# Optimization experiments

Measured on AMD Instinct MI355X. Metric: run time of the kernel, lower is better.

Reference implementation:

```python
import jax, jax.numpy as jnp
import numpy as np

N_NODES = 50000
N_EDGES = 800000
IN_DIM = 16
HID = 128
OUT_DIM = 1
N_LAYERS = 2


def setup_inputs() -> dict:
    key = jax.random.key(0)
    ks = jax.random.split(key, 16)
    s = 0.05
    inp = {
        "edge_feats": jax.random.normal(ks[0], (N_EDGES, IN_DIM), jnp.float32),
        "node_feats": jax.random.normal(ks[1], (N_NODES, 4), jnp.float32),
        "src": jax.random.randint(ks[2], (N_EDGES,), 0, N_NODES, jnp.int32),
        "dst": jax.random.randint(ks[3], (N_EDGES,), 0, N_NODES, jnp.int32),
        # edge_embedding (dead in original forward, kept for faithfulness)
        "W_eemb": jax.random.normal(ks[4], (IN_DIM, HID), jnp.float32) * s,
        "b_eemb": jnp.zeros((HID,), jnp.float32),
        # node_embedding: Linear(4, hidden)
        "W_nemb": jax.random.normal(ks[5], (4, HID), jnp.float32) * s,
        "b_nemb": jnp.zeros((HID,), jnp.float32),
        # stacked GraphConv weights [n_layers, H, H]
        "gnn_W": jax.random.normal(ks[6], (N_LAYERS, HID, HID), jnp.float32) * s,
        "gnn_b": jnp.zeros((N_LAYERS, HID), jnp.float32),
        # output MLP
        "out_W1": jax.random.normal(ks[7], (HID, HID), jnp.float32) * s,
        "out_b1": jnp.zeros((HID,), jnp.float32),
        "out_W2": jax.random.normal(ks[8], (HID, OUT_DIM), jnp.float32) * s,
        "out_b2": jnp.zeros((OUT_DIM,), jnp.float32),
    }
    return inp


def reference(edge_feats, node_feats, src, dst, W_eemb, b_eemb, W_nemb, b_nemb,
              gnn_W, gnn_b, out_W1, out_b1, out_W2, out_b2):
    ones = jnp.ones((src.shape[0],), jnp.float32)
    deg_out = jnp.clip(jax.ops.segment_sum(ones, src, num_segments=N_NODES), 1.0)
    deg_in = jnp.clip(jax.ops.segment_sum(ones, dst, num_segments=N_NODES), 1.0)
    norm_out = deg_out ** -0.5  # [N]
    norm_in = deg_in ** -0.5    # [N]

    # edge_embedding output is dead code in the original forward (overwritten)
    _h_e = edge_feats @ W_eemb + b_eemb

    h = node_feats @ W_nemb + b_nemb  # [N, H]
    for l in range(N_LAYERS):
        # DGL GraphConv norm='both': D_out^{-1/2} gather -> scatter-sum -> D_in^{-1/2} -> W, b
        hs = h * norm_out[:, None]
        agg = jax.ops.segment_sum(hs[src], dst, num_segments=N_NODES)  # [N, H]
        h = agg * norm_in[:, None]
        h = h @ gnn_W[l] + gnn_b[l]
        h = jax.nn.relu(h)

    edge_h = h[src] + h[dst]  # apply_edges UDF, [E, H]
    x = jax.nn.relu(edge_h @ out_W1 + out_b1)
    return x @ out_W2 + out_b2  # [E, OUT_DIM]
```

## Files before the change

kernel.cpp:

```cpp
#include <hip/hip_runtime.h>

#define N_NODES 50000
#define N_EDGES 800000
#define HID 128
#define NB 256
#define NPB 196
#define TP 136

typedef __attribute__((ext_vector_type(8))) short bf16x8;
typedef __attribute__((ext_vector_type(4))) float f32x4;

__device__ __forceinline__ unsigned pack2bf(float a, float b) {
  unsigned ua = __float_as_uint(a);
  ua += 0x7FFFu + ((ua >> 16) & 1u);
  unsigned ub = __float_as_uint(b);
  ub += 0x7FFFu + ((ub >> 16) & 1u);
  return (ua >> 16) | (ub & 0xFFFF0000u);
}
#define BFLO(u) __uint_as_float((u) << 16)
#define BFHI(u) __uint_as_float((u) & 0xFFFF0000u)


__global__ __launch_bounds__(256) void p1_hist_kernel(
    const int* __restrict__ src, const int* __restrict__ dst,
    int* __restrict__ bcnt_d, int* __restrict__ bcnt_s) {
  __shared__ int hd[NB], hs[NB];
  int t = threadIdx.x;
  hd[t] = 0; hs[t] = 0;
  __syncthreads();
  for (int e = blockIdx.x * 256 + t; e < N_EDGES; e += gridDim.x * 256) {
    atomicAdd(&hd[dst[e] / NPB], 1);
    atomicAdd(&hs[src[e] / NPB], 1);
  }
  __syncthreads();
  if (hd[t]) atomicAdd(&bcnt_d[t], hd[t]);
  if (hs[t]) atomicAdd(&bcnt_s[t], hs[t]);
}

__global__ void p2_scan_kernel(const int* __restrict__ bcnt_d, const int* __restrict__ bcnt_s,
                               int* __restrict__ bofs_d, int* __restrict__ bofs_s,
                               int* __restrict__ cur_d, int* __restrict__ cur_s) {
  __shared__ int s[NB];
  int t = threadIdx.x;
  int v = bcnt_d[t];
  s[t] = v;
  __syncthreads();
  for (int o = 1; o < NB; o <<= 1) {
    int x = (t >= o) ? s[t - o] : 0;
    __syncthreads();
    s[t] += x;
    __syncthreads();
  }
  int ofs = s[t] - v;
  bofs_d[t] = ofs; cur_d[t] = ofs;
  if (t == NB - 1) bofs_d[NB] = s[t];
  __syncthreads();
  v = bcnt_s[t];
  s[t] = v;
  __syncthreads();
  for (int o = 1; o < NB; o <<= 1) {
    int x = (t >= o) ? s[t - o] : 0;
    __syncthreads();
    s[t] += x;
    __syncthreads();
  }
  ofs = s[t] - v;
  bofs_s[t] = ofs; cur_s[t] = ofs;
  if (t == NB - 1) bofs_s[NB] = s[t];
}

__global__ __launch_bounds__(256) void p3_scatter_dst_kernel(
    const int* __restrict__ src, const int* __restrict__ dst,
    int* __restrict__ cur_d, int2* __restrict__ sdst) {
  __shared__ int bcnt[NB], bbase[NB];
  int t = threadIdx.x;
  int base = blockIdx.x * 2048;
  bcnt[t] = 0;
  __syncthreads();
  int myb[8], myr[8], mys[8], myp[8];
#pragma unroll
  for (int u = 0; u < 8; ++u) {
    int e = base + u * 256 + t;
    myb[u] = -1;
    if (e < N_EDGES) {
      int d = dst[e];
      int b = d / NPB;
      myb[u] = b;
      myr[u] = atomicAdd(&bcnt[b], 1);
      mys[u] = src[e];
      myp[u] = ((d - b * NPB) << 20) | e;
    }
  }
  __syncthreads();
  int c = bcnt[t];
  if (c) bbase[t] = atomicAdd(&cur_d[t], c);
  __syncthreads();
#pragma unroll
  for (int u = 0; u < 8; ++u) {
    if (myb[u] >= 0) sdst[bbase[myb[u]] + myr[u]] = make_int2(mys[u], myp[u]);
  }
}

__global__ __launch_bounds__(256) void p3_scatter_src_kernel(
    const int* __restrict__ src, int* __restrict__ cur_s, int* __restrict__ ssrc) {
  __shared__ int bcnt[NB], bbase[NB];
  int t = threadIdx.x;
  int base = blockIdx.x * 2048;
  bcnt[t] = 0;
  __syncthreads();
  int myb[8], myr[8], mys[8];
#pragma unroll
  for (int u = 0; u < 8; ++u) {
    int e = base + u * 256 + t;
    myb[u] = -1;
    if (e < N_EDGES) {
      int s = src[e];
      int b = s / NPB;
      myb[u] = b;
      myr[u] = atomicAdd(&bcnt[b], 1);
      mys[u] = s;
    }
  }
  __syncthreads();
  int c = bcnt[t];
  if (c) bbase[t] = atomicAdd(&cur_s[t], c);
  __syncthreads();
#pragma unroll
  for (int u = 0; u < 8; ++u) {
    if (myb[u] >= 0) ssrc[bbase[myb[u]] + myr[u]] = mys[u];
  }
}

__global__ __launch_bounds__(256) void p4_csr_kernel(
    const int2* __restrict__ sdst, const int* __restrict__ bofs_d,
    int* __restrict__ row_ofs, float* __restrict__ norm_in,
    int* __restrict__ csr_src, int* __restrict__ csr_eid) {
  __shared__ int hc[NB], sc[NB], cur[NB];
  int b = blockIdx.x, t = threadIdx.x;
  int base = bofs_d[b], cnt = bofs_d[b + 1] - base;
  hc[t] = 0;
  __syncthreads();
  for (int i = t; i < cnt; i += 256) atomicAdd(&hc[sdst[base + i].y >> 20], 1);
  __syncthreads();
  int v = hc[t];
  sc[t] = v;
  __syncthreads();
  for (int o = 1; o < NB; o <<= 1) {
    int x = (t >= o) ? sc[t - o] : 0;
    __syncthreads();
    sc[t] += x;
    __syncthreads();
  }
  int ofs = sc[t] - v;
  int node = b * NPB + t;
  if (t < NPB && node < N_NODES) {
    row_ofs[node] = base + ofs;
    norm_in[node] = rsqrtf((float)(v < 1 ? 1 : v));
  }
  cur[t] = base + ofs;
  if (b == 0 && t == 0) row_ofs[N_NODES] = N_EDGES;
  __syncthreads();
  for (int i = t; i < cnt; i += 256) {
    int2 e = sdst[base + i];
    int pos = atomicAdd(&cur[e.y >> 20], 1);
    csr_src[pos] = e.x;
    csr_eid[pos] = e.y & 0xFFFFF;
  }
}

__global__ __launch_bounds__(256) void p5_degout_kernel(
    const int* __restrict__ ssrc, const int* __restrict__ bofs_s,
    float* __restrict__ norm_out) {
  __shared__ int hc[NB];
  int b = blockIdx.x, t = threadIdx.x;
  int base = bofs_s[b], cnt = bofs_s[b + 1] - base;
  int lo = b * NPB;
  hc[t] = 0;
  __syncthreads();
  for (int i = t; i < cnt; i += 256) atomicAdd(&hc[ssrc[base + i] - lo], 1);
  __syncthreads();
  int node = lo + t;
  if (t < NPB && node < N_NODES) {
    int v = hc[t];
    norm_out[node] = rsqrtf((float)(v < 1 ? 1 : v));
  }
}

__global__ __launch_bounds__(256) void prep_w_kernel(
    const float* __restrict__ W0, const float* __restrict__ W1,
    short* __restrict__ Wt0, short* __restrict__ Wt1) {
  int t = blockIdx.x * 256 + threadIdx.x;
  if (t < HID * HID) {
    int k = t >> 7, n = t & 127;
    Wt0[n * HID + k] = (short)(pack2bf(W0[t], 0.f) & 0xFFFFu);
    Wt1[n * HID + k] = (short)(pack2bf(W1[t], 0.f) & 0xFFFFu);
  }
}


__global__ __launch_bounds__(256) void agg4_kernel(
    const float4* __restrict__ nf4, const float* __restrict__ no_,
    const int* __restrict__ csr_src, const int* __restrict__ row_ofs,
    float4* __restrict__ agg4, float* __restrict__ sno) {
  int wid = (blockIdx.x * blockDim.x + threadIdx.x) >> 6;
  int lane = threadIdx.x & 63;
  int g = lane >> 4, l = lane & 15;
  int v = wid * 4 + g;
  if (v >= N_NODES) return;
  int beg = row_ofs[v], end = row_ofs[v + 1];
  float ax = 0.f, ay = 0.f, az = 0.f, aw = 0.f, sn = 0.f;
  for (int i = beg + l; i < end; i += 16) {
    int s = csr_src[i];
    float w = no_[s];
    float4 n = nf4[s];
    ax += n.x * w; ay += n.y * w; az += n.z * w; aw += n.w * w;
    sn += w;
  }
#pragma unroll
  for (int o = 1; o < 16; o <<= 1) {
    ax += __shfl_xor(ax, o, 16);
    ay += __shfl_xor(ay, o, 16);
    az += __shfl_xor(az, o, 16);
    aw += __shfl_xor(aw, o, 16);
    sn += __shfl_xor(sn, o, 16);
  }
  if (l == 0) {
    agg4[v] = make_float4(ax, ay, az, aw);
    sno[v] = sn;
  }
}

__global__ __launch_bounds__(256) void gemm_l1_kernel(
    const float4* __restrict__ agg4, const float* __restrict__ sno,
    const float* __restrict__ ni_, const float* __restrict__ no_,
    const float* __restrict__ Wn, const float* __restrict__ bn,
    const float* __restrict__ W0, const float* __restrict__ b0,
    uint4* __restrict__ h1b, int nrows) {
  __shared__ float At[HID * 64];
  __shared__ float Wbuf[32 * HID];
  int t = threadIdx.x;
  int v0 = blockIdx.x * 64;
  {
    int r = t & 63, kg = t >> 6;
    int v = v0 + r;
    float4 a = make_float4(0.f, 0.f, 0.f, 0.f);
    float sn = 0.f, nin = 0.f;
    if (v < nrows) { a = agg4[v]; sn = sno[v]; nin = ni_[v]; }
    for (int kk = 0; kk < 32; ++kk) {
      int k = kg * 32 + kk;
      float val = (a.x * Wn[k] + a.y * Wn[HID + k] + a.z * Wn[2 * HID + k] +
                   a.w * Wn[3 * HID + k] + bn[k] * sn) * nin;
      At[k * 64 + r] = val;
    }
  }
  int c0 = (t >> 4) * 8, r0 = (t & 15) * 4;
  float acc[4][8];
#pragma unroll
  for (int i = 0; i < 4; ++i)
#pragma unroll
    for (int j = 0; j < 8; ++j) acc[i][j] = 0.f;

  for (int kc = 0; kc < HID; kc += 32) {
    __syncthreads();
    {
      const float4* wsrc = (const float4*)(W0 + kc * HID);
      float4* wdst = (float4*)Wbuf;
#pragma unroll
      for (int i = 0; i < 4; ++i) wdst[i * 256 + t] = wsrc[i * 256 + t];
    }
    __syncthreads();
#pragma unroll 4
    for (int kk = 0; kk < 32; ++kk) {
      float4 av = *(const float4*)&At[(kc + kk) * 64 + r0];
      float4 w0v = *(const float4*)&Wbuf[kk * HID + c0];
      float4 w1v = *(const float4*)&Wbuf[kk * HID + c0 + 4];
      float ar[4] = {av.x, av.y, av.z, av.w};
      float wv[8] = {w0v.x, w0v.y, w0v.z, w0v.w, w1v.x, w1v.y, w1v.z, w1v.w};
#pragma unroll
      for (int i = 0; i < 4; ++i)
#pragma unroll
        for (int j = 0; j < 8; ++j) acc[i][j] += ar[i] * wv[j];
    }
  }
  float bb[8];
  {
    float4 b0v = *(const float4*)&b0[c0];
    float4 b1v = *(const float4*)&b0[c0 + 4];
    bb[0] = b0v.x; bb[1] = b0v.y; bb[2] = b0v.z; bb[3] = b0v.w;
    bb[4] = b1v.x; bb[5] = b1v.y; bb[6] = b1v.z; bb[7] = b1v.w;
  }
#pragma unroll
  for (int i = 0; i < 4; ++i) {
    int v = v0 + r0 + i;
    if (v < nrows) {
      float nov = no_[v];
      float o[8];
#pragma unroll
      for (int j = 0; j < 8; ++j) o[j] = fmaxf(acc[i][j] + bb[j], 0.f) * nov;
      uint4 pk;
      pk.x = pack2bf(o[0], o[1]); pk.y = pack2bf(o[2], o[3]);
      pk.z = pack2bf(o[4], o[5]); pk.w = pack2bf(o[6], o[7]);
      h1b[(size_t)v * 16 + (c0 >> 3)] = pk;
    }
  }
}

__global__ __launch_bounds__(256) void aggregate_kernel(
    const uint4* __restrict__ hb, const int* __restrict__ row_ofs,
    const int* __restrict__ csr_src, const float* __restrict__ ni_,
    uint4* __restrict__ Ab) {
  int v = (blockIdx.x * blockDim.x + threadIdx.x) >> 6;
  int lane = threadIdx.x & 63;
  if (v >= N_NODES) return;
  int beg = row_ofs[v], end = row_ofs[v + 1];
  int g = lane >> 4, l = lane & 15;
  float acc[8];
#pragma unroll
  for (int j = 0; j < 8; ++j) acc[j] = 0.f;
  for (int i = beg; i < end; i += 16) {
    int ii[4]; float mm[4]; int ss[4];
#pragma unroll
    for (int u = 0; u < 4; ++u) {
      ii[u] = i + 4 * u + g;
      bool q = ii[u] < end;
      mm[u] = q ? 1.f : 0.f;
      ss[u] = csr_src[q ? ii[u] : beg];
    }
    uint4 X[4];
#pragma unroll
    for (int u = 0; u < 4; ++u) X[u] = hb[(size_t)ss[u] * 16 + l];
#pragma unroll
    for (int u = 0; u < 4; ++u) {
      acc[0] += BFLO(X[u].x) * mm[u]; acc[1] += BFHI(X[u].x) * mm[u];
      acc[2] += BFLO(X[u].y) * mm[u]; acc[3] += BFHI(X[u].y) * mm[u];
      acc[4] += BFLO(X[u].z) * mm[u]; acc[5] += BFHI(X[u].z) * mm[u];
      acc[6] += BFLO(X[u].w) * mm[u]; acc[7] += BFHI(X[u].w) * mm[u];
    }
  }
#pragma unroll
  for (int j = 0; j < 8; ++j) {
    acc[j] += __shfl_xor(acc[j], 16, 64);
    acc[j] += __shfl_xor(acc[j], 32, 64);
  }
  if (g == 0) {
    float n = ni_[v];
    uint4 pk;
    pk.x = pack2bf(acc[0] * n, acc[1] * n);
    pk.y = pack2bf(acc[2] * n, acc[3] * n);
    pk.z = pack2bf(acc[4] * n, acc[5] * n);
    pk.w = pack2bf(acc[6] * n, acc[7] * n);
    Ab[(size_t)v * 16 + l] = pk;
  }
}

__global__ __launch_bounds__(256) void gemm_dual_mfma(
    const short* __restrict__ Ab, const short* __restrict__ Wt0,
    const float* __restrict__ b0, const short* __restrict__ Wt1,
    short* __restrict__ yb, int nrows) {
  __shared__ short T1s[4][16 * TP];
  int t = threadIdx.x;
  int w = t >> 6, lane = t & 63;
  int m16 = lane & 15, quad = lane >> 4;
  int v0 = blockIdx.x * 64;
  int row = v0 + w * 16 + m16;
  bool rvalid = row < nrows;
  int rc = rvalid ? row : (nrows - 1);

  bf16x8 xfr[4];
  {
    const bf16x8* Ar = (const bf16x8*)(Ab + (size_t)rc * HID);
#pragma unroll
    for (int kc = 0; kc < 4; ++kc) xfr[kc] = Ar[kc * 4 + quad];
  }
  f32x4 acc[8];
#pragma unroll
  for (int nt = 0; nt < 8; ++nt) {
    acc[nt][0] = 0.f; acc[nt][1] = 0.f; acc[nt][2] = 0.f; acc[nt][3] = 0.f;
  }
#pragma unroll
  for (int nt = 0; nt < 8; ++nt) {
    const bf16x8* Wr = (const bf16x8*)(Wt0 + (size_t)(nt * 16 + m16) * HID);
#pragma unroll
    for (int kc = 0; kc < 4; ++kc)
      acc[nt] = __builtin_amdgcn_mfma_f32_16x16x32_bf16(Wr[kc * 4 + quad], xfr[kc],
                                                        acc[nt], 0, 0, 0);
  }
  short* T1w = &T1s[w][0];
#pragma unroll
  for (int nt = 0; nt < 8; ++nt) {
    int nb = nt * 16 + quad * 4;
    float4 bv = *(const float4*)&b0[nb];
    float r0 = fmaxf(acc[nt][0] + bv.x, 0.f);
    float r1 = fmaxf(acc[nt][1] + bv.y, 0.f);
    float r2 = fmaxf(acc[nt][2] + bv.z, 0.f);
    float r3 = fmaxf(acc[nt][3] + bv.w, 0.f);
    uint2 pk;
    pk.x = pack2bf(r0, r1);
    pk.y = pack2bf(r2, r3);
    *(uint2*)&T1w[m16 * TP + nb] = pk;
    acc[nt][0] = 0.f; acc[nt][1] = 0.f; acc[nt][2] = 0.f; acc[nt][3] = 0.f;
  }
  __syncthreads();
  bf16x8 tfr[4];
#pragma unroll
  for (int kc = 0; kc < 4; ++kc)
    tfr[kc] = *(const bf16x8*)&T1w[m16 * TP + kc * 32 + quad * 8];
#pragma unroll
  for (int nt = 0; nt < 8; ++nt) {
    const bf16x8* Wr = (const bf16x8*)(Wt1 + (size_t)(nt * 16 + m16) * HID);
#pragma unroll
    for (int kc = 0; kc < 4; ++kc)
      acc[nt] = __builtin_amdgcn_mfma_f32_16x16x32_bf16(Wr[kc * 4 + quad], tfr[kc],
                                                        acc[nt], 0, 0, 0);
  }
  if (rvalid) {
#pragma unroll
    for (int nt = 0; nt < 8; ++nt) {
      int nb = nt * 16 + quad * 4;
      uint2 pk;
      pk.x = pack2bf(acc[nt][0], acc[nt][1]);
      pk.y = pack2bf(acc[nt][2], acc[nt][3]);
      *(uint2*)(yb + (size_t)row * HID + nb) = pk;
    }
  }
}

__global__ __launch_bounds__(256) void edge_out_kernel(
    const int* __restrict__ csr_src, const int* __restrict__ csr_eid,
    const int* __restrict__ row_ofs, const uint4* __restrict__ yb,
    const float* __restrict__ b1, const float* __restrict__ w2,
    const float* __restrict__ b2, float* __restrict__ out) {
  int v = (blockIdx.x * blockDim.x + threadIdx.x) >> 6;
  int lane = threadIdx.x & 63;
  if (v >= N_NODES) return;
  int beg = row_ofs[v], end = row_ofs[v + 1];
  if (beg >= end) return;
  int g = lane >> 4, l = lane & 15;
  uint4 D = yb[(size_t)v * 16 + l];
  float d[8] = {BFLO(D.x), BFHI(D.x), BFLO(D.y), BFHI(D.y),
                BFLO(D.z), BFHI(D.z), BFLO(D.w), BFHI(D.w)};
  {
    float4 q0 = ((const float4*)b1)[l * 2], q1 = ((const float4*)b1)[l * 2 + 1];
    d[0] += q0.x; d[1] += q0.y; d[2] += q0.z; d[3] += q0.w;
    d[4] += q1.x; d[5] += q1.y; d[6] += q1.z; d[7] += q1.w;
  }
  float w[8];
  {
    float4 q0 = ((const float4*)w2)[l * 2], q1 = ((const float4*)w2)[l * 2 + 1];
    w[0] = q0.x; w[1] = q0.y; w[2] = q0.z; w[3] = q0.w;
    w[4] = q1.x; w[5] = q1.y; w[6] = q1.z; w[7] = q1.w;
  }
  float ob2 = b2[0];
  for (int i = beg; i < end; i += 16) {
    int ii[4]; bool qq[4]; int ss[4];
#pragma unroll
    for (int u = 0; u < 4; ++u) {
      ii[u] = i + 4 * u + g;
      qq[u] = ii[u] < end;
      ss[u] = csr_src[qq[u] ? ii[u] : beg];
    }
    uint4 A[4];
#pragma unroll
    for (int u = 0; u < 4; ++u) A[u] = yb[(size_t)ss[u] * 16 + l];
#pragma unroll
    for (int u = 0; u < 4; ++u) {
      float p = fmaxf(BFLO(A[u].x) + d[0], 0.f) * w[0] +
                fmaxf(BFHI(A[u].x) + d[1], 0.f) * w[1] +
                fmaxf(BFLO(A[u].y) + d[2], 0.f) * w[2] +
                fmaxf(BFHI(A[u].y) + d[3], 0.f) * w[3] +
                fmaxf(BFLO(A[u].z) + d[4], 0.f) * w[4] +
                fmaxf(BFHI(A[u].z) + d[5], 0.f) * w[5] +
                fmaxf(BFLO(A[u].w) + d[6], 0.f) * w[6] +
                fmaxf(BFHI(A[u].w) + d[7], 0.f) * w[7];
      p += __shfl_down(p, 8, 16);
      p += __shfl_down(p, 4, 16);
      p += __shfl_down(p, 2, 16);
      p += __shfl_down(p, 1, 16);
      if (l == 0 && qq[u]) out[csr_eid[ii[u]]] = p + ob2;
    }
  }
}

extern "C" void kernel_launch(void* const* d_in, const int* in_sizes, int n_in,
                              void* d_out, int out_size, void* d_ws, size_t ws_size,
                              hipStream_t stream) {
  const float* node_feats = (const float*)d_in[1];
  const int*   src        = (const int*)d_in[2];
  const int*   dst        = (const int*)d_in[3];
  const float* W_nemb     = (const float*)d_in[6];
  const float* b_nemb     = (const float*)d_in[7];
  const float* gnn_W      = (const float*)d_in[8];
  const float* gnn_b      = (const float*)d_in[9];
  const float* out_W1     = (const float*)d_in[10];
  const float* out_b1     = (const float*)d_in[11];
  const float* out_W2     = (const float*)d_in[12];
  const float* out_b2     = (const float*)d_in[13];
  float* out = (float*)d_out;

  size_t off = 0;
  char* base = (char*)d_ws;
  auto alloc = [&](size_t nbytes) -> char* {
    off = (off + 255) & ~(size_t)255;
    char* p = base + off;
    off += nbytes;
    return p;
  };
  int*    bcnt2    = (int*)alloc(2 * NB * 4);
  int*    bofs_d   = (int*)alloc((NB + 1) * 4);
  int*    bofs_s   = (int*)alloc((NB + 1) * 4);
  int*    cur_d    = (int*)alloc(NB * 4);
  int*    cur_s    = (int*)alloc(NB * 4);
  float*  norm_out = (float*)alloc(N_NODES * 4);
  float*  norm_in  = (float*)alloc(N_NODES * 4);
  int*    row_ofs  = (int*)alloc((N_NODES + 1) * 4);
  int*    csr_src  = (int*)alloc((size_t)N_EDGES * 4);
  int*    csr_eid  = (int*)alloc((size_t)N_EDGES * 4);
  float4* agg4     = (float4*)alloc((size_t)N_NODES * 16);
  float*  sno      = (float*)alloc(N_NODES * 4);
  short*  Wt0      = (short*)alloc((size_t)HID * HID * 2);
  short*  Wt1      = (short*)alloc((size_t)HID * HID * 2);
  uint4*  h1b      = (uint4*)alloc((size_t)N_NODES * HID * 2);
  short*  Ab       = (short*)alloc((size_t)N_NODES * HID * 2);
  short*  ybs      = (short*)alloc((size_t)N_NODES * HID * 2);
  int2*   sdst     = (int2*)Ab;
  int*    ssrc     = (int*)ybs;
  int*    bcnt_d   = bcnt2;
  int*    bcnt_s   = bcnt2 + NB;
  (void)ws_size; (void)n_in; (void)in_sizes; (void)out_size;

  hipMemsetAsync(bcnt2, 0, 2 * NB * 4, stream);
  prep_w_kernel<<<(HID * HID + 255) / 256, 256, 0, stream>>>(
      gnn_W + (size_t)HID * HID, out_W1, Wt0, Wt1);
  p1_hist_kernel<<<128, 256, 0, stream>>>(src, dst, bcnt_d, bcnt_s);
  p2_scan_kernel<<<1, 256, 0, stream>>>(bcnt_d, bcnt_s, bofs_d, bofs_s, cur_d, cur_s);
  p3_scatter_dst_kernel<<<(N_EDGES + 2047) / 2048, 256, 0, stream>>>(src, dst, cur_d, sdst);
  p3_scatter_src_kernel<<<(N_EDGES + 2047) / 2048, 256, 0, stream>>>(src, cur_s, ssrc);
  p4_csr_kernel<<<NB, 256, 0, stream>>>(sdst, bofs_d, row_ofs, norm_in, csr_src, csr_eid);
  p5_degout_kernel<<<NB, 256, 0, stream>>>(ssrc, bofs_s, norm_out);

  agg4_kernel<<<(N_NODES * 16 + 255) / 256, 256, 0, stream>>>(
      (const float4*)node_feats, norm_out, csr_src, row_ofs, agg4, sno);
  gemm_l1_kernel<<<(N_NODES + 63) / 64, 256, 0, stream>>>(
      agg4, sno, norm_in, norm_out, W_nemb, b_nemb, gnn_W, gnn_b, h1b, N_NODES);

  aggregate_kernel<<<(N_NODES * 64 + 255) / 256, 256, 0, stream>>>(
      h1b, row_ofs, csr_src, norm_in, (uint4*)Ab);

  gemm_dual_mfma<<<(N_NODES + 63) / 64, 256, 0, stream>>>(
      Ab, Wt0, gnn_b + HID, Wt1, ybs, N_NODES);

  edge_out_kernel<<<(N_NODES * 64 + 255) / 256, 256, 0, stream>>>(
      csr_src, csr_eid, row_ofs, (const uint4*)ybs, out_b1, out_W2, out_b2, out);
}
```

Before: 320.3 us.

## Use MFMA for layer-1 GEMM, fuse scatter kernels, vectorize aggregate loops

The fp32 LDS-tiled layer-1 GEMM is replaced by a bf16 MFMA kernel that builds its A fragments in registers from the 4-wide aggregate, using a pre-transposed bf16 copy of the weight. The two scatter kernels for dst and src buckets are merged into one pass over the edges, saving a launch and a second read of src. The aggregate kernel now uses a zeroed sentinel row instead of mask multiplies for out-of-range edges, and the aggregate and edge-output inner loops are rewritten with float2 helpers. The weight goes through bf16 rounding before the first GEMM, which slightly lowers precision there.

Result: faster. 312.7 us (-2.4%).

```diff
diff --git a/kernel.cpp b/kernel.cpp
--- a/kernel.cpp
+++ b/kernel.cpp
@@ -19,6 +19,19 @@
 }
 #define BFLO(u) __uint_as_float((u) << 16)
 #define BFHI(u) __uint_as_float((u) & 0xFFFF0000u)
+
+__device__ __forceinline__ float2 unpk(unsigned u) {
+  return make_float2(BFLO(u), BFHI(u));
+}
+__device__ __forceinline__ float2 f2add(float2 a, float2 b) {
+  return make_float2(a.x + b.x, a.y + b.y);
+}
+__device__ __forceinline__ float2 f2max0(float2 a) {
+  return make_float2(fmaxf(a.x, 0.f), fmaxf(a.y, 0.f));
+}
+__device__ __forceinline__ float2 f2fma(float2 a, float2 b, float2 c) {
+  return make_float2(fmaf(a.x, b.x, c.x), fmaf(a.y, b.y, c.y));
+}
 
 
 __global__ __launch_bounds__(256) void p1_hist_kernel(
@@ -69,65 +82,46 @@
   if (t == NB - 1) bofs_s[NB] = s[t];
 }
 
-__global__ __launch_bounds__(256) void p3_scatter_dst_kernel(
+__global__ __launch_bounds__(256) void p3_scatter_both_kernel(
     const int* __restrict__ src, const int* __restrict__ dst,
-    int* __restrict__ cur_d, int2* __restrict__ sdst) {
-  __shared__ int bcnt[NB], bbase[NB];
+    int* __restrict__ cur_d, int* __restrict__ cur_s,
+    int2* __restrict__ sdst, int* __restrict__ ssrc) {
+  __shared__ int bcd[NB], bbd[NB], bcs[NB], bbs[NB];
   int t = threadIdx.x;
   int base = blockIdx.x * 2048;
-  bcnt[t] = 0;
-  __syncthreads();
-  int myb[8], myr[8], mys[8], myp[8];
+  bcd[t] = 0; bcs[t] = 0;
+  __syncthreads();
+  int mybd[8], myrd[8], mys[8], myp[8], mybs[8], myrs[8];
 #pragma unroll
   for (int u = 0; u < 8; ++u) {
     int e = base + u * 256 + t;
-    myb[u] = -1;
+    mybd[u] = -1;
     if (e < N_EDGES) {
-      int d = dst[e];
-      int b = d / NPB;
-      myb[u] = b;
-      myr[u] = atomicAdd(&bcnt[b], 1);
-      mys[u] = src[e];
-      myp[u] = ((d - b * NPB) << 20) | e;
-    }
-  }
-  __syncthreads();
-  int c = bcnt[t];
-  if (c) bbase[t] = atomicAdd(&cur_d[t], c);
+      int s = src[e], d = dst[e];
+      int bd = d / NPB;
+      mybd[u] = bd;
+      myrd[u] = atomicAdd(&bcd[bd], 1);
+      mys[u] = s;
+      myp[u] = ((d - bd * NPB) << 20) | e;
+      int bs = s / NPB;
+      mybs[u] = bs;
+      myrs[u] = atomicAdd(&bcs[bs], 1);
+    }
+  }
+  __syncthreads();
+  {
+    int cd = bcd[t];
+    if (cd) bbd[t] = atomicAdd(&cur_d[t], cd);
+    int cs = bcs[t];
+    if (cs) bbs[t] = atomicAdd(&cur_s[t], cs);
+  }
   __syncthreads();
 #pragma unroll
   for (int u = 0; u < 8; ++u) {
-    if (myb[u] >= 0) sdst[bbase[myb[u]] + myr[u]] = make_int2(mys[u], myp[u]);
-  }
-}
-
-__global__ __launch_bounds__(256) void p3_scatter_src_kernel(
-    const int* __restrict__ src, int* __restrict__ cur_s, int* __restrict__ ssrc) {
-  __shared__ int bcnt[NB], bbase[NB];
-  int t = threadIdx.x;
-  int base = blockIdx.x * 2048;
-  bcnt[t] = 0;
-  __syncthreads();
-  int myb[8], myr[8], mys[8];
-#pragma unroll
-  for (int u = 0; u < 8; ++u) {
-    int e = base + u * 256 + t;
-    myb[u] = -1;
-    if (e < N_EDGES) {
-      int s = src[e];
-      int b = s / NPB;
-      myb[u] = b;
-      myr[u] = atomicAdd(&bcnt[b], 1);
-      mys[u] = s;
-    }
-  }
-  __syncthreads();
-  int c = bcnt[t];
-  if (c) bbase[t] = atomicAdd(&cur_s[t], c);
-  __syncthreads();
-#pragma unroll
-  for (int u = 0; u < 8; ++u) {
-    if (myb[u] >= 0) ssrc[bbase[myb[u]] + myr[u]] = mys[u];
+    if (mybd[u] >= 0) {
+      sdst[bbd[mybd[u]] + myrd[u]] = make_int2(mys[u], myp[u]);
+      ssrc[bbs[mybs[u]] + myrs[u]] = mys[u];
+    }
   }
 }
 
@@ -187,13 +181,15 @@
 }
 
 __global__ __launch_bounds__(256) void prep_w_kernel(
-    const float* __restrict__ W0, const float* __restrict__ W1,
-    short* __restrict__ Wt0, short* __restrict__ Wt1) {
+    const float* __restrict__ Wa, const float* __restrict__ Wb,
+    const float* __restrict__ Wc, short* __restrict__ Wta,
+    short* __restrict__ Wtb, short* __restrict__ Wtc) {
   int t = blockIdx.x * 256 + threadIdx.x;
   if (t < HID * HID) {
     int k = t >> 7, n = t & 127;
-    Wt0[n * HID + k] = (short)(pack2bf(W0[t], 0.f) & 0xFFFFu);
-    Wt1[n * HID + k] = (short)(pack2bf(W1[t], 0.f) & 0xFFFFu);
+    Wta[n * HID + k] = (short)(pack2bf(Wa[t], 0.f) & 0xFFFFu);
+    Wtb[n * HID + k] = (short)(pack2bf(Wb[t], 0.f) & 0xFFFFu);
+    Wtc[n * HID + k] = (short)(pack2bf(Wc[t], 0.f) & 0xFFFFu);
   }
 }
 
@@ -230,77 +226,65 @@
   }
 }
 
-__global__ __launch_bounds__(256) void gemm_l1_kernel(
+__global__ __launch_bounds__(256) void gemm_l1_mfma(
     const float4* __restrict__ agg4, const float* __restrict__ sno,
     const float* __restrict__ ni_, const float* __restrict__ no_,
     const float* __restrict__ Wn, const float* __restrict__ bn,
-    const float* __restrict__ W0, const float* __restrict__ b0,
-    uint4* __restrict__ h1b, int nrows) {
-  __shared__ float At[HID * 64];
-  __shared__ float Wbuf[32 * HID];
+    const short* __restrict__ Wt0, const float* __restrict__ b0,
+    short* __restrict__ h1b, int nrows) {
   int t = threadIdx.x;
+  int w = t >> 6, lane = t & 63;
+  int m16 = lane & 15, quad = lane >> 4;
   int v0 = blockIdx.x * 64;
-  {
-    int r = t & 63, kg = t >> 6;
-    int v = v0 + r;
-    float4 a = make_float4(0.f, 0.f, 0.f, 0.f);
-    float sn = 0.f, nin = 0.f;
-    if (v < nrows) { a = agg4[v]; sn = sno[v]; nin = ni_[v]; }
-    for (int kk = 0; kk < 32; ++kk) {
-      int k = kg * 32 + kk;
-      float val = (a.x * Wn[k] + a.y * Wn[HID + k] + a.z * Wn[2 * HID + k] +
-                   a.w * Wn[3 * HID + k] + bn[k] * sn) * nin;
-      At[k * 64 + r] = val;
-    }
-  }
-  int c0 = (t >> 4) * 8, r0 = (t & 15) * 4;
-  float acc[4][8];
-#pragma unroll
-  for (int i = 0; i < 4; ++i)
-#pragma unroll
-    for (int j = 0; j < 8; ++j) acc[i][j] = 0.f;
-
-  for (int kc = 0; kc < HID; kc += 32) {
-    __syncthreads();
-    {
-      const float4* wsrc = (const float4*)(W0 + kc * HID);
-      float4* wdst = (float4*)Wbuf;
-#pragma unroll
-      for (int i = 0; i < 4; ++i) wdst[i * 256 + t] = wsrc[i * 256 + t];
-    }
-    __syncthreads();
-#pragma unroll 4
-    for (int kk = 0; kk < 32; ++kk) {
-      float4 av = *(const float4*)&At[(kc + kk) * 64 + r0];
-      float4 w0v = *(const float4*)&Wbuf[kk * HID + c0];
-      float4 w1v = *(const float4*)&Wbuf[kk * HID + c0 + 4];
-      float ar[4] = {av.x, av.y, av.z, av.w};
-      float wv[8] = {w0v.x, w0v.y, w0v.z, w0v.w, w1v.x, w1v.y, w1v.z, w1v.w};
-#pragma unroll
-      for (int i = 0; i < 4; ++i)
-#pragma unroll
-        for (int j = 0; j < 8; ++j) acc[i][j] += ar[i] * wv[j];
-    }
-  }
-  float bb[8];
-  {
-    float4 b0v = *(const float4*)&b0[c0];
-    float4 b1v = *(const float4*)&b0[c0 + 4];
-    bb[0] = b0v.x; bb[1] = b0v.y; bb[2] = b0v.z; bb[3] = b0v.w;
-    bb[4] = b1v.x; bb[5] = b1v.y; bb[6] = b1v.z; bb[7] = b1v.w;
-  }
-#pragma unroll
-  for (int i = 0; i < 4; ++i) {
-    int v = v0 + r0 + i;
-    if (v < nrows) {
-      float nov = no_[v];
-      float o[8];
-#pragma unroll
-      for (int j = 0; j < 8; ++j) o[j] = fmaxf(acc[i][j] + bb[j], 0.f) * nov;
-      uint4 pk;
-      pk.x = pack2bf(o[0], o[1]); pk.y = pack2bf(o[2], o[3]);
-      pk.z = pack2bf(o[4], o[5]); pk.w = pack2bf(o[6], o[7]);
-      h1b[(size_t)v * 16 + (c0 >> 3)] = pk;
+  int row = v0 + w * 16 + m16;
+  bool rvalid = row < nrows;
+  int rc = rvalid ? row : (nrows - 1);
+  float4 a = agg4[rc];
+  float sn = sno[rc], nin = ni_[rc];
+
+  bf16x8 xfr[4];
+#pragma unroll
+  for (int kc = 0; kc < 4; ++kc) {
+    union { unsigned u[4]; bf16x8 v; } cv;
+#pragma unroll
+    for (int jj = 0; jj < 4; ++jj) {
+      int k0 = kc * 32 + quad * 8 + jj * 2;
+      float x0 = (a.x * Wn[k0] + a.y * Wn[HID + k0] + a.z * Wn[2 * HID + k0] +
+                  a.w * Wn[3 * HID + k0] + bn[k0] * sn) * nin;
+      int k1 = k0 + 1;
+      float x1 = (a.x * Wn[k1] + a.y * Wn[HID + k1] + a.z * Wn[2 * HID + k1] +
+                  a.w * Wn[3 * HID + k1] + bn[k1] * sn) * nin;
+      cv.u[jj] = pack2bf(x0, x1);
+    }
+    xfr[kc] = cv.v;
+  }
+  f32x4 acc[8];
+#pragma unroll
+  for (int nt = 0; nt < 8; ++nt) {
+    acc[nt][0] = 0.f; acc[nt][1] = 0.f; acc[nt][2] = 0.f; acc[nt][3] = 0.f;
+  }
+#pragma unroll
+  for (int nt = 0; nt < 8; ++nt) {
+    const bf16x8* Wr = (const bf16x8*)(Wt0 + (size_t)(nt * 16 + m16) * HID);
+#pragma unroll
+    for (int kc = 0; kc < 4; ++kc)
+      acc[nt] = __builtin_amdgcn_mfma_f32_16x16x32_bf16(Wr[kc * 4 + quad], xfr[kc],
+                                                        acc[nt], 0, 0, 0);
+  }
+  if (rvalid) {
+    float nov = no_[row];
+#pragma unroll
+    for (int nt = 0; nt < 8; ++nt) {
+      int nb = nt * 16 + quad * 4;
+      float4 bv = *(const float4*)&b0[nb];
+      float r0 = fmaxf(acc[nt][0] + bv.x, 0.f) * nov;
+      float r1 = fmaxf(acc[nt][1] + bv.y, 0.f) * nov;
+      float r2 = fmaxf(acc[nt][2] + bv.z, 0.f) * nov;
+      float r3 = fmaxf(acc[nt][3] + bv.w, 0.f) * nov;
+      uint2 pk;
+      pk.x = pack2bf(r0, r1);
+      pk.y = pack2bf(r2, r3);
+      *(uint2*)(h1b + (size_t)row * HID + nb) = pk;
     }
   }
 }
@@ -314,41 +298,41 @@
   if (v >= N_NODES) return;
   int beg = row_ofs[v], end = row_ofs[v + 1];
   int g = lane >> 4, l = lane & 15;
-  float acc[8];
-#pragma unroll
-  for (int j = 0; j < 8; ++j) acc[j] = 0.f;
+  float2 acc2[4];
+#pragma unroll
+  for (int j = 0; j < 4; ++j) acc2[j] = make_float2(0.f, 0.f);
   for (int i = beg; i < end; i += 16) {
-    int ii[4]; float mm[4]; int ss[4];
+    int ss[4];
 #pragma unroll
     for (int u = 0; u < 4; ++u) {
-      ii[u] = i + 4 * u + g;
-      bool q = ii[u] < end;
-      mm[u] = q ? 1.f : 0.f;
-      ss[u] = csr_src[q ? ii[u] : beg];
+      int ii = i + 4 * u + g;
+      ss[u] = (ii < end) ? csr_src[ii] : N_NODES;
     }
     uint4 X[4];
 #pragma unroll
     for (int u = 0; u < 4; ++u) X[u] = hb[(size_t)ss[u] * 16 + l];
 #pragma unroll
     for (int u = 0; u < 4; ++u) {
-      acc[0] += BFLO(X[u].x) * mm[u]; acc[1] += BFHI(X[u].x) * mm[u];
-      acc[2] += BFLO(X[u].y) * mm[u]; acc[3] += BFHI(X[u].y) * mm[u];
-      acc[4] += BFLO(X[u].z) * mm[u]; acc[5] += BFHI(X[u].z) * mm[u];
-      acc[6] += BFLO(X[u].w) * mm[u]; acc[7] += BFHI(X[u].w) * mm[u];
-    }
-  }
-#pragma unroll
-  for (int j = 0; j < 8; ++j) {
-    acc[j] += __shfl_xor(acc[j], 16, 64);
-    acc[j] += __shfl_xor(acc[j], 32, 64);
+      acc2[0] = f2add(acc2[0], unpk(X[u].x));
+      acc2[1] = f2add(acc2[1], unpk(X[u].y));
+      acc2[2] = f2add(acc2[2], unpk(X[u].z));
+      acc2[3] = f2add(acc2[3], unpk(X[u].w));
+    }
+  }
+#pragma unroll
+  for (int j = 0; j < 4; ++j) {
+    acc2[j].x += __shfl_xor(acc2[j].x, 16, 64);
+    acc2[j].x += __shfl_xor(acc2[j].x, 32, 64);
+    acc2[j].y += __shfl_xor(acc2[j].y, 16, 64);
+    acc2[j].y += __shfl_xor(acc2[j].y, 32, 64);
   }
   if (g == 0) {
     float n = ni_[v];
     uint4 pk;
-    pk.x = pack2bf(acc[0] * n, acc[1] * n);
-    pk.y = pack2bf(acc[2] * n, acc[3] * n);
-    pk.z = pack2bf(acc[4] * n, acc[5] * n);
-    pk.w = pack2bf(acc[6] * n, acc[7] * n);
+    pk.x = pack2bf(acc2[0].x * n, acc2[0].y * n);
+    pk.y = pack2bf(acc2[1].x * n, acc2[1].y * n);
+    pk.z = pack2bf(acc2[2].x * n, acc2[2].y * n);
+    pk.w = pack2bf(acc2[3].x * n, acc2[3].y * n);
     Ab[(size_t)v * 16 + l] = pk;
   }
 }
@@ -436,20 +420,15 @@
   int beg = row_ofs[v], end = row_ofs[v + 1];
   if (beg >= end) return;
   int g = lane >> 4, l = lane & 15;
+  const float2* b12 = (const float2*)b1;
+  const float2* w22 = (const float2*)w2;
   uint4 D = yb[(size_t)v * 16 + l];
-  float d[8] = {BFLO(D.x), BFHI(D.x), BFLO(D.y), BFHI(D.y),
-                BFLO(D.z), BFHI(D.z), BFLO(D.w), BFHI(D.w)};
-  {
-    float4 q0 = ((const float4*)b1)[l * 2], q1 = ((const float4*)b1)[l * 2 + 1];
-    d[0] += q0.x; d[1] += q0.y; d[2] += q0.z; d[3] += q0.w;
-    d[4] += q1.x; d[5] += q1.y; d[6] += q1.z; d[7] += q1.w;
-  }
-  float w[8];
-  {
-    float4 q0 = ((const float4*)w2)[l * 2], q1 = ((const float4*)w2)[l * 2 + 1];
-    w[0] = q0.x; w[1] = q0.y; w[2] = q0.z; w[3] = q0.w;
-    w[4] = q1.x; w[5] = q1.y; w[6] = q1.z; w[7] = q1.w;
-  }
+  float2 d0 = f2add(unpk(D.x), b12[l * 4 + 0]);
+  float2 d1 = f2add(unpk(D.y), b12[l * 4 + 1]);
+  float2 d2 = f2add(unpk(D.z), b12[l * 4 + 2]);
+  float2 d3 = f2add(unpk(D.w), b12[l * 4 + 3]);
+  float2 w0 = w22[l * 4 + 0], w1 = w22[l * 4 + 1];
+  float2 w2v = w22[l * 4 + 2], w3 = w22[l * 4 + 3];
   float ob2 = b2[0];
   for (int i = beg; i < end; i += 16) {
     int ii[4]; bool qq[4]; int ss[4];
@@ -464,14 +443,13 @@
     for (int u = 0; u < 4; ++u) A[u] = yb[(size_t)ss[u] * 16 + l];
 #pragma unroll
     for (int u = 0; u < 4; ++u) {
-      float p = fmaxf(BFLO(A[u].x) + d[0], 0.f) * w[0] +
-                fmaxf(BFHI(A[u].x) + d[1], 0.f) * w[1] +
-                fmaxf(BFLO(A[u].y) + d[2], 0.f) * w[2] +
-                fmaxf(BFHI(A[u].y) + d[3], 0.f) * w[3] +
-                fmaxf(BFLO(A[u].z) + d[4], 0.f) * w[4] +
-                fmaxf(BFHI(A[u].z) + d[5], 0.f) * w[5] +
-                fmaxf(BFLO(A[u].w) + d[6], 0.f) * w[6] +
-                fmaxf(BFHI(A[u].w) + d[7], 0.f) * w[7];
+      float2 p2;
+      p2.x = 0.f; p2.y = 0.f;
+      p2 = f2fma(f2max0(f2add(unpk(A[u].x), d0)), w0, p2);
+      p2 = f2fma(f2max0(f2add(unpk(A[u].y), d1)), w1, p2);
+      p2 = f2fma(f2max0(f2add(unpk(A[u].z), d2)), w2v, p2);
+      p2 = f2fma(f2max0(f2add(unpk(A[u].w), d3)), w3, p2);
+      float p = p2.x + p2.y;
       p += __shfl_down(p, 8, 16);
       p += __shfl_down(p, 4, 16);
       p += __shfl_down(p, 2, 16);
@@ -517,9 +495,10 @@
   int*    csr_eid  = (int*)alloc((size_t)N_EDGES * 4);
   float4* agg4     = (float4*)alloc((size_t)N_NODES * 16);
   float*  sno      = (float*)alloc(N_NODES * 4);
-  short*  Wt0      = (short*)alloc((size_t)HID * HID * 2);
-  short*  Wt1      = (short*)alloc((size_t)HID * HID * 2);
-  uint4*  h1b      = (uint4*)alloc((size_t)N_NODES * HID * 2);
+  short*  Wta      = (short*)alloc((size_t)HID * HID * 2);
+  short*  Wtb      = (short*)alloc((size_t)HID * HID * 2);
+  short*  Wtc     = (short*)alloc((size_t)HID * HID * 2);
+  short*  h1b      = (short*)alloc((size_t)(N_NODES + 1) * HID * 2);
   short*  Ab       = (short*)alloc((size_t)N_NODES * HID * 2);
   short*  ybs      = (short*)alloc((size_t)N_NODES * HID * 2);
   int2*   sdst     = (int2*)Ab;
@@ -529,25 +508,26 @@
   (void)ws_size; (void)n_in; (void)in_sizes; (void)out_size;
 
   hipMemsetAsync(bcnt2, 0, 2 * NB * 4, stream);
+  hipMemsetAsync(h1b + (size_t)N_NODES * HID, 0, HID * 2, stream);
   prep_w_kernel<<<(HID * HID + 255) / 256, 256, 0, stream>>>(
-      gnn_W + (size_t)HID * HID, out_W1, Wt0, Wt1);
+      gnn_W, gnn_W + (size_t)HID * HID, out_W1, Wta, Wtb, Wtc);
   p1_hist_kernel<<<128, 256, 0, stream>>>(src, dst, bcnt_d, bcnt_s);
   p2_scan_kernel<<<1, 256, 0, stream>>>(bcnt_d, bcnt_s, bofs_d, bofs_s, cur_d, cur_s);
-  p3_scatter_dst_kernel<<<(N_EDGES + 2047) / 2048, 256, 0, stream>>>(src, dst, cur_d, sdst);
-  p3_scatter_src_kernel<<<(N_EDGES + 2047) / 2048, 256, 0, stream>>>(src, cur_s, ssrc);
+  p3_scatter_both_kernel<<<(N_EDGES + 2047) / 2048, 256, 0, stream>>>(
+      src, dst, cur_d, cur_s, sdst, ssrc);
   p4_csr_kernel<<<NB, 256, 0, stream>>>(sdst, bofs_d, row_ofs, norm_in, csr_src, csr_eid);
   p5_degout_kernel<<<NB, 256, 0, stream>>>(ssrc, bofs_s, norm_out);
 
   agg4_kernel<<<(N_NODES * 16 + 255) / 256, 256, 0, stream>>>(
       (const float4*)node_feats, norm_out, csr_src, row_ofs, agg4, sno);
-  gemm_l1_kernel<<<(N_NODES + 63) / 64, 256, 0, stream>>>(
-      agg4, sno, norm_in, norm_out, W_nemb, b_nemb, gnn_W, gnn_b, h1b, N_NODES);
+  gemm_l1_mfma<<<(N_NODES + 63) / 64, 256, 0, stream>>>(
+      agg4, sno, norm_in, norm_out, W_nemb, b_nemb, Wta, gnn_b, h1b, N_NODES);
 
   aggregate_kernel<<<(N_NODES * 64 + 255) / 256, 256, 0, stream>>>(
-      h1b, row_ofs, csr_src, norm_in, (uint4*)Ab);
+      (const uint4*)h1b, row_ofs, csr_src, norm_in, (uint4*)Ab);
 
   gemm_dual_mfma<<<(N_NODES + 63) / 64, 256, 0, stream>>>(
-      Ab, Wt0, gnn_b + HID, Wt1, ybs, N_NODES);
+      Ab, Wtb, gnn_b + HID, Wtc, ybs, N_NODES);
 
   edge_out_kernel<<<(N_NODES * 64 + 255) / 256, 256, 0, stream>>>(
       csr_src, csr_eid, row_ofs, (const uint4*)ybs, out_b1, out_W2, out_b2, out);
```
